# Kernel optimization log

Hardware: AMD Instinct MI355X
Metric: run time of the kernel (lower is better)

Reference implementation:

```python
import jax, jax.numpy as jnp
import numpy as np

B, N, D = 4096, 64, 128

def setup_inputs() -> dict:
    key = jax.random.key(0)
    ks = jax.random.split(key, 5)
    return {
        "stu_emb": jax.random.normal(ks[0], (B, D), jnp.float32),
        "concept_emb": jax.random.normal(ks[1], (B, D), jnp.float32),
        "neighbor_emb": jax.random.normal(ks[2], (B, N, D), jnp.float32),
        # Linear(2D -> D) for stu_concept_integration (xavier-like scale)
        "Ws": jax.random.normal(ks[3], (2 * D, D), jnp.float32) * (2.0 / (3 * D)) ** 0.5,
        "bs": jnp.full((D,), 0.1, jnp.float32),
        # Linear(2D -> 1) for concept_neighbor_weight
        "Ww": jax.random.normal(ks[4], (2 * D, 1), jnp.float32) * (2.0 / (2 * D + 1)) ** 0.5,
        "bw": jnp.full((1,), 0.1, jnp.float32),
    }


def reference(stu_emb, concept_emb, neighbor_emb, Ws, bs, Ww, bw):
    # Masks: 1 where the (first) concatenated input is nonzero along features
    dt = stu_emb.dtype
    mask_s = (jnp.sum(stu_emb, -1, keepdims=True) != 0).astype(dt)[:, None, :]      # [B,1,1]
    mask_c = (jnp.sum(concept_emb, -1, keepdims=True) != 0).astype(dt)[:, None, :]  # [B,1,1]

    # Split concat-linear into two halves so the broadcasted half is computed once
    Ws_a, Ws_b = Ws[:D], Ws[D:]   # [D,D] each
    Ww_a, Ww_b = Ww[:D], Ww[D:]   # [D,1] each

    stu_part = stu_emb @ Ws_a            # [B,D]
    con_part = concept_emb @ Ws_b        # [B,D]
    nbr_part = neighbor_emb @ Ws_b       # [B,N,D]

    # neighbor attention weights: Linear(2D->1)(cat(concept_ext, neighbor)) * mask_c
    w = (concept_emb @ Ww_a)[:, None, :] + neighbor_emb @ Ww_b + bw  # [B,N,1]
    w = w * mask_c
    w = jax.nn.softmax(w, axis=-2)  # softmax over neighbor axis

    # stu integrated with neighbors / with the original concept, masked by stu mask
    integ_n = (stu_part[:, None, :] + nbr_part + bs) * mask_s            # [B,N,D]
    integ_o = (stu_part[:, None, :] + con_part[:, None, :] + bs) * mask_s  # [B,N,D] (broadcast)

    # combine over neighbor axis and average the two branches
    y = jnp.sum(integ_o + w * integ_n, axis=-2) / 2  # [B,D]
    return y
```

## Files before the change

kernel.cpp:

```cpp
#include <hip/hip_runtime.h>

#define BB 4096
#define NN 64
#define DD 128
#define G  4

__global__ __launch_bounds__(256, 4) void kFused(
    const float* __restrict__ stu,
    const float* __restrict__ conc,
    const float* __restrict__ nbr,
    const float* __restrict__ Ws,
    const float* __restrict__ bs,
    const float* __restrict__ Ww,
    float* __restrict__ y)
{
    const int t    = threadIdx.x;
    const int lane = t & 63;
    const int cg   = t & 31;
    const int g8   = t >> 5;
    const int wv   = t >> 6;
    const int b0   = blockIdx.x * G;

    __shared__ float logits[NN];
    __shared__ __align__(16) float u[G][2 * DD];
    __shared__ __align__(16) float part[4 * DD];
    __shared__ __align__(16) float scratch[8 * G * DD];

    const float4 wb = reinterpret_cast<const float4*>(Ww + DD)[cg];

    float msk0 = 0.f, msk1 = 0.f, msk2 = 0.f, msk3 = 0.f;

    const float4* nb4 = reinterpret_cast<const float4*>(nbr);
    float4 val[8], valn[8];
#pragma unroll
    for (int i = 0; i < 8; ++i) val[i] = nb4[(size_t)b0 * 2048 + t + 256 * i];

#pragma unroll
    for (int g = 0; g < G; ++g) {
        const int b = b0 + g;

        if (g < G - 1) {
#pragma unroll
            for (int i = 0; i < 8; ++i)
                valn[i] = nb4[(size_t)(b + 1) * 2048 + t + 256 * i];
        }

        float cv0 = conc[(size_t)b * DD + lane];
        float cv1 = conc[(size_t)b * DD + 64 + lane];
        float sv0 = stu [(size_t)b * DD + lane];
        float sv1 = stu [(size_t)b * DD + 64 + lane];
        float cs = cv0 + cv1, ss = sv0 + sv1;
#pragma unroll
        for (int o = 1; o < 64; o <<= 1) {
            cs += __shfl_xor(cs, o);
            ss += __shfl_xor(ss, o);
        }
        const float mg = (ss != 0.0f) ? 0.5f : 0.0f;
        if      (g == 0) msk0 = mg;
        else if (g == 1) msk1 = mg;
        else if (g == 2) msk2 = mg;
        else             msk3 = mg;

        if (t < 64) {
            u[g][t]           = 65.0f * sv0;
            u[g][t + 64]      = 65.0f * sv1;
            u[g][DD + t]      = 64.0f * cv0;
            u[g][DD + 64 + t] = 64.0f * cv1;
        }

#pragma unroll
        for (int i = 0; i < 8; ++i) {
            float x = val[i].x * wb.x + val[i].y * wb.y
                    + val[i].z * wb.z + val[i].w * wb.w;
            x += __shfl_xor(x, 1);
            x += __shfl_xor(x, 2);
            x += __shfl_xor(x, 4);
            x += __shfl_xor(x, 8);
            x += __shfl_xor(x, 16);
            if (cg == 0) logits[g8 + 8 * i] = x;
        }
        __syncthreads();

        float l = logits[lane];
        float m = l;
        m = fmaxf(m, __shfl_xor(m, 1));
        m = fmaxf(m, __shfl_xor(m, 2));
        m = fmaxf(m, __shfl_xor(m, 4));
        m = fmaxf(m, __shfl_xor(m, 8));
        m = fmaxf(m, __shfl_xor(m, 16));
        m = fmaxf(m, __shfl_xor(m, 32));
        float e = __expf(l - m);
        float sden = e;
        sden += __shfl_xor(sden, 1);
        sden += __shfl_xor(sden, 2);
        sden += __shfl_xor(sden, 4);
        sden += __shfl_xor(sden, 8);
        sden += __shfl_xor(sden, 16);
        sden += __shfl_xor(sden, 32);
        const float wlane = (cs != 0.0f) ? (e / sden) : (1.0f / 64.0f);

        float4 a = {0.f, 0.f, 0.f, 0.f};
#pragma unroll
        for (int i = 0; i < 8; ++i) {
            float w = __shfl(wlane, g8 + 8 * i);
            a.x += w * val[i].x; a.y += w * val[i].y;
            a.z += w * val[i].z; a.w += w * val[i].w;
        }
        a.x += __shfl_xor(a.x, 32);
        a.y += __shfl_xor(a.y, 32);
        a.z += __shfl_xor(a.z, 32);
        a.w += __shfl_xor(a.w, 32);
        if (lane < 32)
            reinterpret_cast<float4*>(part)[wv * 32 + cg] = a;
        __syncthreads();

        if (t < DD) {
            float vsum = part[t] + part[DD + t] + part[2 * DD + t] + part[3 * DD + t];
            u[g][DD + t] += vsum;
        }

        if (g < G - 1) {
#pragma unroll
            for (int i = 0; i < 8; ++i) val[i] = valn[i];
        }
    }
    __syncthreads();

    float4 acc0 = {0,0,0,0}, acc1 = {0,0,0,0}, acc2 = {0,0,0,0}, acc3 = {0,0,0,0};
    const float4* Ws4 = reinterpret_cast<const float4*>(Ws);
#pragma unroll 4
    for (int j = 0; j < 32; ++j) {
        const int k = g8 * 32 + j;
        float4 wvv = Ws4[k * 32 + cg];
        float u0 = u[0][k], u1 = u[1][k], u2 = u[2][k], u3 = u[3][k];
        acc0.x += u0 * wvv.x; acc0.y += u0 * wvv.y; acc0.z += u0 * wvv.z; acc0.w += u0 * wvv.w;
        acc1.x += u1 * wvv.x; acc1.y += u1 * wvv.y; acc1.z += u1 * wvv.z; acc1.w += u1 * wvv.w;
        acc2.x += u2 * wvv.x; acc2.y += u2 * wvv.y; acc2.z += u2 * wvv.z; acc2.w += u2 * wvv.w;
        acc3.x += u3 * wvv.x; acc3.y += u3 * wvv.y; acc3.z += u3 * wvv.z; acc3.w += u3 * wvv.w;
    }
    {
        float4* pr = reinterpret_cast<float4*>(scratch);
        pr[(g8 * G + 0) * 32 + cg] = acc0;
        pr[(g8 * G + 1) * 32 + cg] = acc1;
        pr[(g8 * G + 2) * 32 + cg] = acc2;
        pr[(g8 * G + 3) * 32 + cg] = acc3;
    }
    __syncthreads();

    const int r1 = t >> 7;
    const int c  = t & 127;
    const float mA = r1 ? msk1 : msk0;
    const float mB = r1 ? msk3 : msk2;
    float sA = 0.0f, sB = 0.0f;
#pragma unroll
    for (int k2 = 0; k2 < 8; ++k2) {
        sA += scratch[(k2 * G + r1) * DD + c];
        sB += scratch[(k2 * G + 2 + r1) * DD + c];
    }
    const float bc = bs[c];
    y[(size_t)(b0 + r1) * DD + c]     = (sA + 65.0f * bc) * mA;
    y[(size_t)(b0 + 2 + r1) * DD + c] = (sB + 65.0f * bc) * mB;
}

extern "C" void kernel_launch(void* const* d_in, const int* in_sizes, int n_in,
                              void* d_out, int out_size, void* d_ws, size_t ws_size,
                              hipStream_t stream) {
    const float* stu  = (const float*)d_in[0];
    const float* conc = (const float*)d_in[1];
    const float* nbr  = (const float*)d_in[2];
    const float* Ws   = (const float*)d_in[3];
    const float* bs   = (const float*)d_in[4];
    const float* Ww   = (const float*)d_in[5];
    float* y = (float*)d_out;

    kFused<<<BB / G, 256, 0, stream>>>(stu, conc, nbr, Ws, bs, Ww, y);
}
```

Measured before the change: 35.85 us.

## Halve rows per block, drop register prefetch, use nontemporal neighbor loads

Cuts the rows per block from 4 to 2, which doubles the grid to 2048 blocks. It removes the manual double-buffered register prefetch of the next row's neighbor tile and loads each row with nontemporal loads instead. It also drops the occupancy hint from the launch bounds. The aim is to hide memory latency through more resident blocks and lower register pressure rather than software prefetch, and to avoid polluting the cache with streamed data. The cost is that the Ws matrix is now reread by twice as many blocks, and each block no longer overlaps its own loads with compute.

After: 37.67 us. 5.1% more time.

```diff
diff --git a/kernel.cpp b/kernel.cpp
--- a/kernel.cpp
+++ b/kernel.cpp
@@ -3,9 +3,11 @@
 #define BB 4096
 #define NN 64
 #define DD 128
-#define G  4
+#define G  2
 
-__global__ __launch_bounds__(256, 4) void kFused(
+typedef float fx4 __attribute__((ext_vector_type(4)));
+
+__global__ __launch_bounds__(256) void kFused(
     const float* __restrict__ stu,
     const float* __restrict__ conc,
     const float* __restrict__ nbr,
@@ -22,28 +24,23 @@
     const int b0   = blockIdx.x * G;
 
     __shared__ float logits[NN];
+    __shared__ __align__(16) float part[4 * DD];
     __shared__ __align__(16) float u[G][2 * DD];
-    __shared__ __align__(16) float part[4 * DD];
     __shared__ __align__(16) float scratch[8 * G * DD];
 
     const float4 wb = reinterpret_cast<const float4*>(Ww + DD)[cg];
+    float msk0 = 0.f, msk1 = 0.f;
 
-    float msk0 = 0.f, msk1 = 0.f, msk2 = 0.f, msk3 = 0.f;
-
-    const float4* nb4 = reinterpret_cast<const float4*>(nbr);
-    float4 val[8], valn[8];
-#pragma unroll
-    for (int i = 0; i < 8; ++i) val[i] = nb4[(size_t)b0 * 2048 + t + 256 * i];
+    const fx4* nb4 = reinterpret_cast<const fx4*>(nbr);
 
 #pragma unroll
     for (int g = 0; g < G; ++g) {
         const int b = b0 + g;
 
-        if (g < G - 1) {
+        fx4 val[8];
 #pragma unroll
-            for (int i = 0; i < 8; ++i)
-                valn[i] = nb4[(size_t)(b + 1) * 2048 + t + 256 * i];
-        }
+        for (int i = 0; i < 8; ++i)
+            val[i] = __builtin_nontemporal_load(&nb4[(size_t)b * 2048 + t + 256 * i]);
 
         float cv0 = conc[(size_t)b * DD + lane];
         float cv1 = conc[(size_t)b * DD + 64 + lane];
@@ -56,14 +53,11 @@
             ss += __shfl_xor(ss, o);
         }
         const float mg = (ss != 0.0f) ? 0.5f : 0.0f;
-        if      (g == 0) msk0 = mg;
-        else if (g == 1) msk1 = mg;
-        else if (g == 2) msk2 = mg;
-        else             msk3 = mg;
+        if (g == 0) msk0 = mg; else msk1 = mg;
 
         if (t < 64) {
             u[g][t]           = 65.0f * sv0;
-            u[g][t + 64]      = 65.0f * sv1;
+            u[g][64 + t]      = 65.0f * sv1;
             u[g][DD + t]      = 64.0f * cv0;
             u[g][DD + 64 + t] = 64.0f * cv1;
         }
@@ -114,52 +108,37 @@
             reinterpret_cast<float4*>(part)[wv * 32 + cg] = a;
         __syncthreads();
 
-        if (t < DD) {
-            float vsum = part[t] + part[DD + t] + part[2 * DD + t] + part[3 * DD + t];
-            u[g][DD + t] += vsum;
-        }
-
-        if (g < G - 1) {
-#pragma unroll
-            for (int i = 0; i < 8; ++i) val[i] = valn[i];
-        }
+        if (t < DD)
+            u[g][DD + t] += part[t] + part[DD + t] + part[2 * DD + t] + part[3 * DD + t];
     }
     __syncthreads();
 
-    float4 acc0 = {0,0,0,0}, acc1 = {0,0,0,0}, acc2 = {0,0,0,0}, acc3 = {0,0,0,0};
+    float4 acc0 = {0,0,0,0}, acc1 = {0,0,0,0};
     const float4* Ws4 = reinterpret_cast<const float4*>(Ws);
 #pragma unroll 4
     for (int j = 0; j < 32; ++j) {
         const int k = g8 * 32 + j;
-        float4 wvv = Ws4[k * 32 + cg];
-        float u0 = u[0][k], u1 = u[1][k], u2 = u[2][k], u3 = u[3][k];
-        acc0.x += u0 * wvv.x; acc0.y += u0 * wvv.y; acc0.z += u0 * wvv.z; acc0.w += u0 * wvv.w;
-        acc1.x += u1 * wvv.x; acc1.y += u1 * wvv.y; acc1.z += u1 * wvv.z; acc1.w += u1 * wvv.w;
-        acc2.x += u2 * wvv.x; acc2.y += u2 * wvv.y; acc2.z += u2 * wvv.z; acc2.w += u2 * wvv.w;
-        acc3.x += u3 * wvv.x; acc3.y += u3 * wvv.y; acc3.z += u3 * wvv.z; acc3.w += u3 * wvv.w;
+        float4 wq = Ws4[k * 32 + cg];
+        float u0 = u[0][k], u1 = u[1][k];
+        acc0.x += u0 * wq.x; acc0.y += u0 * wq.y; acc0.z += u0 * wq.z; acc0.w += u0 * wq.w;
+        acc1.x += u1 * wq.x; acc1.y += u1 * wq.y; acc1.z += u1 * wq.z; acc1.w += u1 * wq.w;
     }
     {
         float4* pr = reinterpret_cast<float4*>(scratch);
         pr[(g8 * G + 0) * 32 + cg] = acc0;
         pr[(g8 * G + 1) * 32 + cg] = acc1;
-        pr[(g8 * G + 2) * 32 + cg] = acc2;
-        pr[(g8 * G + 3) * 32 + cg] = acc3;
     }
     __syncthreads();
-
-    const int r1 = t >> 7;
-    const int c  = t & 127;
-    const float mA = r1 ? msk1 : msk0;
-    const float mB = r1 ? msk3 : msk2;
-    float sA = 0.0f, sB = 0.0f;
+    {
+        const int r = t >> 7;
+        const int c = t & 127;
+        float s = 0.0f;
 #pragma unroll
-    for (int k2 = 0; k2 < 8; ++k2) {
-        sA += scratch[(k2 * G + r1) * DD + c];
-        sB += scratch[(k2 * G + 2 + r1) * DD + c];
+        for (int k2 = 0; k2 < 8; ++k2)
+            s += scratch[(k2 * G + r) * DD + c];
+        const float mr = r ? msk1 : msk0;
+        y[(size_t)(b0 + r) * DD + c] = (s + 65.0f * bs[c]) * mr;
     }
-    const float bc = bs[c];
-    y[(size_t)(b0 + r1) * DD + c]     = (sA + 65.0f * bc) * mA;
-    y[(size_t)(b0 + 2 + r1) * DD + c] = (sB + 65.0f * bc) * mB;
 }
 
 extern "C" void kernel_launch(void* const* d_in, const int* in_sizes, int n_in,
```
